# Performance work log

Hardware: AMD Instinct MI355X
Metric: run time of the kernel (lower is better)

## Reference

```python
import jax, jax.numpy as jnp
import numpy as np

N, B, C = 16384, 8, 256

def setup_inputs() -> dict:
    key = jax.random.key(0)
    k1, k2, k3, k4 = jax.random.split(key, 4)
    x = jax.random.normal(k1, (N, B, C), dtype=jnp.float32)
    mask = jax.random.randint(k2, (B, N), 0, 2, dtype=jnp.int32)      # 1 = padding
    fg_gt = jax.random.randint(k3, (N, B), 0, 2, dtype=jnp.int32)     # 1 = foreground gt
    W = jax.random.normal(k4, (C, C), dtype=jnp.float32) * (1.0 / np.sqrt(C))
    b = jnp.zeros((C,), dtype=jnp.float32)
    return {"x": x, "mask": mask, "fg_gt": fg_gt, "W": W, "b": b}

def reference(x, mask, fg_gt, W, b):
    # valid tokens: ~mask, permuted (B,N) -> (N,B)
    valid = (1 - mask.T).astype(x.dtype)                 # (N, B)
    m = (fg_gt != 0).astype(x.dtype) * valid             # gt_fg_token_mask, (N, B)
    # The per-batch gather -> Linear+ReLU -> scatter is equivalent to a
    # full batched GEMM followed by a masked select (linear is per-token).
    y = jax.nn.relu(jnp.einsum('nbc,dc->nbd', x, W) + b) # (N, B, C)
    x_new = x * (1.0 - m)[..., None] + y * m[..., None]
    return x_new, m
```

## Files before the change

kernel.cpp:

```cpp
#include <hip/hip_runtime.h>
#include <hip/hip_bf16.h>

#define N_TOK 16384
#define B_DIM 8
#define C_DIM 256
#define M_ROWS (N_TOK * B_DIM)
#define BM 32

typedef __attribute__((ext_vector_type(8))) short short8;
typedef __attribute__((ext_vector_type(4))) float f32x4;

__device__ __forceinline__ unsigned short f2bf(float f) {
    union { float f; unsigned u; } v; v.f = f;
    unsigned r = v.u + 0x7fffu + ((v.u >> 16) & 1u);
    return (unsigned short)(r >> 16);
}

__device__ __forceinline__ float bf2f(unsigned short h) {
    union { unsigned u; float f; } v; v.u = ((unsigned)h) << 16;
    return v.f;
}

__device__ __forceinline__ unsigned cvt_pk(float a, float b) {
    unsigned r;
    asm("v_cvt_pk_bf16_f32 %0, %1, %2" : "=v"(r) : "v"(a), "v"(b));
    return r;
}

__global__ __launch_bounds__(256)
void prep_kernel(const int* __restrict__ mask, const int* __restrict__ fg,
                 const float* __restrict__ W, unsigned short* __restrict__ Wf,
                 float* __restrict__ m_out) {
    int i = blockIdx.x * 256 + threadIdx.x;
    if (i < C_DIM * C_DIM) {
        int d = i >> 8;
        int c = i & 255;
        int ctile = d >> 4;
        int k8    = c >> 5;
        int lane  = ((c >> 3) & 3) * 16 + (d & 15);
        int r     = c & 7;
        Wf[((ctile * 8 + k8) * 64 + lane) * 8 + r] = f2bf(W[i]);
    }
    if (i < M_ROWS) {
        int b = i & (B_DIM - 1);
        int n = i >> 3;
        m_out[i] = (fg[i] != 0) ? (1.0f - (float)mask[b * N_TOK + n]) : 0.0f;
    }
}

__global__ __launch_bounds__(256, 6)
void mlp_kernel(const float* __restrict__ x, const unsigned short* __restrict__ Wf,
                const float* __restrict__ bias, const float* __restrict__ m,
                float* __restrict__ out) {
    __shared__ unsigned short lds_x[BM * C_DIM];

    const int t    = threadIdx.x;
    const int row0 = blockIdx.x * BM;

    #pragma unroll
    for (int j = 0; j < 4; ++j) {
        int ci  = j * 256 + t;
        int row = ci >> 5;
        int cc  = (ci & 31) * 8;
        const float4* p = (const float4*)(x + (size_t)(row0 + row) * C_DIM + cc);
        float4 a0 = p[0];
        float4 a1 = p[1];
        int4 pk;
        pk.x = (int)cvt_pk(a0.x, a0.y);
        pk.y = (int)cvt_pk(a0.z, a0.w);
        pk.z = (int)cvt_pk(a1.x, a1.y);
        pk.w = (int)cvt_pk(a1.z, a1.w);
        int byte = (row * 512 + cc * 2) ^ ((row & 7) << 4);
        *(int4*)((char*)lds_x + byte) = pk;
    }
    __syncthreads();

    const int lane = t & 63;
    const int wid  = t >> 6;
    const int col0 = wid * 64;
    const int lr   = lane & 15;
    const int kb   = (lane >> 4) * 8;
    const int rsub = (lane >> 4) * 4;

    f32x4 acc[2][4];
    #pragma unroll
    for (int i = 0; i < 2; ++i)
        #pragma unroll
        for (int j = 0; j < 4; ++j) acc[i][j] = (f32x4){0.f, 0.f, 0.f, 0.f};

    const short8* wfb = (const short8*)Wf + (size_t)wid * 4 * 8 * 64 + lane;

    #pragma unroll
    for (int k8 = 0; k8 < 8; ++k8) {
        short8 bf[4];
        #pragma unroll
        for (int ct = 0; ct < 4; ++ct)
            bf[ct] = wfb[(ct * 8 + k8) * 64];
        short8 af[2];
        #pragma unroll
        for (int rt = 0; rt < 2; ++rt) {
            int row  = rt * 16 + lr;
            int byte = (row * 512 + (k8 * 32 + kb) * 2) ^ ((row & 7) << 4);
            af[rt] = *(const short8*)((const char*)lds_x + byte);
        }
        #pragma unroll
        for (int rt = 0; rt < 2; ++rt)
            #pragma unroll
            for (int ct = 0; ct < 4; ++ct)
                acc[rt][ct] = __builtin_amdgcn_mfma_f32_16x16x32_bf16(
                    af[rt], bf[ct], acc[rt][ct], 0, 0, 0);
    }

    float bv[4];
    #pragma unroll
    for (int ct = 0; ct < 4; ++ct) bv[ct] = bias[col0 + ct * 16 + lr];

    #pragma unroll
    for (int rt = 0; rt < 2; ++rt) {
        float4 mreg = *(const float4*)(m + row0 + rt * 16 + rsub);
        #pragma unroll
        for (int r = 0; r < 4; ++r) {
            int lrow = rt * 16 + rsub + r;
            float mv = (r == 0) ? mreg.x : (r == 1) ? mreg.y
                     : (r == 2) ? mreg.z : mreg.w;
            size_t grow = (size_t)row0 + lrow;
            #pragma unroll
            for (int ct = 0; ct < 4; ++ct) {
                int col = col0 + ct * 16 + lr;
                float y = fmaxf(acc[rt][ct][r] + bv[ct], 0.0f);
                int bo = (lrow * 512 + col * 2) ^ ((lrow & 7) << 4);
                float xv = bf2f(*(const unsigned short*)((const char*)lds_x + bo));
                out[grow * C_DIM + col] = (mv != 0.0f) ? y : xv;
            }
        }
    }
}

extern "C" void kernel_launch(void* const* d_in, const int* in_sizes, int n_in,
                              void* d_out, int out_size, void* d_ws, size_t ws_size,
                              hipStream_t stream) {
    const float* x    = (const float*)d_in[0];
    const int*   mask = (const int*)d_in[1];
    const int*   fg   = (const int*)d_in[2];
    const float* W    = (const float*)d_in[3];
    const float* b    = (const float*)d_in[4];

    float* out   = (float*)d_out;
    float* m_out = out + (size_t)M_ROWS * C_DIM;
    unsigned short* Wf = (unsigned short*)d_ws;

    prep_kernel<<<M_ROWS / 256, 256, 0, stream>>>(mask, fg, W, Wf, m_out);
    mlp_kernel<<<M_ROWS / BM, 256, 0, stream>>>(x, Wf, b, m_out, out);
}
```

Measured before the change: 61.84 us.

## Make MLP kernel persistent with double-buffered direct-to-LDS loads and register-resident W

Each block now processes 8 row tiles with 512 threads. It keeps its slice of the bf16 weights in registers across tiles and prefetches the next tile of fp32 x into a second LDS buffer via global_load_lds while computing the current one. The fp32 tile is converted to bf16 at fragment-read time, and the passthrough value is read as exact fp32 from LDS. This aims to overlap HBM loads with MFMA and stores and to drop repeated weight reloads, at the cost of doubled LDS use and reliance on hand-tuned vmcnt waits.

```diff
diff --git a/kernel.cpp b/kernel.cpp
--- a/kernel.cpp
+++ b/kernel.cpp
@@ -6,6 +6,8 @@
 #define C_DIM 256
 #define M_ROWS (N_TOK * B_DIM)
 #define BM 32
+#define TPB 8
+#define GRID 512
 
 typedef __attribute__((ext_vector_type(8))) short short8;
 typedef __attribute__((ext_vector_type(4))) float f32x4;
@@ -16,15 +18,16 @@
     return (unsigned short)(r >> 16);
 }
 
-__device__ __forceinline__ float bf2f(unsigned short h) {
-    union { unsigned u; float f; } v; v.u = ((unsigned)h) << 16;
-    return v.f;
-}
-
 __device__ __forceinline__ unsigned cvt_pk(float a, float b) {
     unsigned r;
     asm("v_cvt_pk_bf16_f32 %0, %1, %2" : "=v"(r) : "v"(a), "v"(b));
     return r;
+}
+
+__device__ __forceinline__ void gload_lds16(const void* g, void* l) {
+    __builtin_amdgcn_global_load_lds(
+        (const __attribute__((address_space(1))) void*)g,
+        (__attribute__((address_space(3))) void*)l, 16, 0, 0);
 }
 
 __global__ __launch_bounds__(256)
@@ -48,91 +51,118 @@
     }
 }
 
-__global__ __launch_bounds__(256, 6)
+__global__ __launch_bounds__(512, 4)
 void mlp_kernel(const float* __restrict__ x, const unsigned short* __restrict__ Wf,
                 const float* __restrict__ bias, const float* __restrict__ m,
                 float* __restrict__ out) {
-    __shared__ unsigned short lds_x[BM * C_DIM];
+    __shared__ float lds[2][BM * C_DIM];
 
     const int t    = threadIdx.x;
-    const int row0 = blockIdx.x * BM;
-
-    #pragma unroll
-    for (int j = 0; j < 4; ++j) {
-        int ci  = j * 256 + t;
-        int row = ci >> 5;
-        int cc  = (ci & 31) * 8;
-        const float4* p = (const float4*)(x + (size_t)(row0 + row) * C_DIM + cc);
-        float4 a0 = p[0];
-        float4 a1 = p[1];
-        int4 pk;
-        pk.x = (int)cvt_pk(a0.x, a0.y);
-        pk.y = (int)cvt_pk(a0.z, a0.w);
-        pk.z = (int)cvt_pk(a1.x, a1.y);
-        pk.w = (int)cvt_pk(a1.z, a1.w);
-        int byte = (row * 512 + cc * 2) ^ ((row & 7) << 4);
-        *(int4*)((char*)lds_x + byte) = pk;
-    }
-    __syncthreads();
-
     const int lane = t & 63;
     const int wid  = t >> 6;
-    const int col0 = wid * 64;
     const int lr   = lane & 15;
     const int kb   = (lane >> 4) * 8;
     const int rsub = (lane >> 4) * 4;
 
-    f32x4 acc[2][4];
+    const int tile0 = blockIdx.x * TPB;
+
+    short8 wreg[2][8];
     #pragma unroll
-    for (int i = 0; i < 2; ++i)
+    for (int c2 = 0; c2 < 2; ++c2)
         #pragma unroll
-        for (int j = 0; j < 4; ++j) acc[i][j] = (f32x4){0.f, 0.f, 0.f, 0.f};
+        for (int k8 = 0; k8 < 8; ++k8)
+            wreg[c2][k8] = ((const short8*)Wf)[((wid * 2 + c2) * 8 + k8) * 64 + lane];
+    #pragma unroll
+    for (int c2 = 0; c2 < 2; ++c2)
+        #pragma unroll
+        for (int k8 = 0; k8 < 8; ++k8)
+            asm volatile("" : "+v"(wreg[c2][k8]));
 
-    const short8* wfb = (const short8*)Wf + (size_t)wid * 4 * 8 * 64 + lane;
+    float bv[2];
+    #pragma unroll
+    for (int c2 = 0; c2 < 2; ++c2) bv[c2] = bias[wid * 32 + c2 * 16 + lr];
 
-    #pragma unroll
-    for (int k8 = 0; k8 < 8; ++k8) {
-        short8 bf[4];
+    auto stage = [&](int buf, int tile) {
+        const char* xb = (const char*)x + (size_t)tile * BM * 1024;
         #pragma unroll
-        for (int ct = 0; ct < 4; ++ct)
-            bf[ct] = wfb[(ct * 8 + k8) * 64];
-        short8 af[2];
+        for (int r = 0; r < 4; ++r) {
+            int row = wid * 4 + r;
+            gload_lds16(xb + row * 1024 + ((lane * 16) ^ ((row & 7) << 4)),
+                        (char*)&lds[buf][0] + row * 1024);
+        }
+    };
+
+    float4 mA, mB, mA_n, mB_n;
+    stage(0, tile0);
+    mA = *(const float4*)(m + tile0 * BM + rsub);
+    mB = *(const float4*)(m + tile0 * BM + 16 + rsub);
+
+    for (int tt = 0; tt < TPB; ++tt) {
+        const int tile = tile0 + tt;
+        const int cur  = tt & 1;
+
+        if (tt == 0) asm volatile("s_waitcnt vmcnt(0)" ::: "memory");
+        else         asm volatile("s_waitcnt vmcnt(16)" ::: "memory");
+        __builtin_amdgcn_s_barrier();
+
+        if (tt + 1 < TPB) {
+            stage(cur ^ 1, tile + 1);
+            mA_n = *(const float4*)(m + (tile + 1) * BM + rsub);
+            mB_n = *(const float4*)(m + (tile + 1) * BM + 16 + rsub);
+        }
+
+        const char* Lc = (const char*)&lds[cur][0];
+        f32x4 acc[2][2];
+        #pragma unroll
+        for (int i = 0; i < 2; ++i)
+            #pragma unroll
+            for (int j = 0; j < 2; ++j) acc[i][j] = (f32x4){0.f, 0.f, 0.f, 0.f};
+
+        #pragma unroll
+        for (int k8 = 0; k8 < 8; ++k8) {
+            short8 af[2];
+            #pragma unroll
+            for (int rt = 0; rt < 2; ++rt) {
+                int row  = rt * 16 + lr;
+                int sz   = (row & 7) << 4;
+                int base = row * 1024 + (k8 * 32 + kb) * 4;
+                float4 f0 = *(const float4*)(Lc + (base ^ sz));
+                float4 f1 = *(const float4*)(Lc + ((base + 16) ^ sz));
+                int4 pk;
+                pk.x = (int)cvt_pk(f0.x, f0.y);
+                pk.y = (int)cvt_pk(f0.z, f0.w);
+                pk.z = (int)cvt_pk(f1.x, f1.y);
+                pk.w = (int)cvt_pk(f1.z, f1.w);
+                af[rt] = *(const short8*)&pk;
+            }
+            #pragma unroll
+            for (int rt = 0; rt < 2; ++rt)
+                #pragma unroll
+                for (int c2 = 0; c2 < 2; ++c2)
+                    acc[rt][c2] = __builtin_amdgcn_mfma_f32_16x16x32_bf16(
+                        af[rt], wreg[c2][k8], acc[rt][c2], 0, 0, 0);
+        }
+
         #pragma unroll
         for (int rt = 0; rt < 2; ++rt) {
-            int row  = rt * 16 + lr;
-            int byte = (row * 512 + (k8 * 32 + kb) * 2) ^ ((row & 7) << 4);
-            af[rt] = *(const short8*)((const char*)lds_x + byte);
-        }
-        #pragma unroll
-        for (int rt = 0; rt < 2; ++rt)
+            float4 mr = rt ? mB : mA;
             #pragma unroll
-            for (int ct = 0; ct < 4; ++ct)
-                acc[rt][ct] = __builtin_amdgcn_mfma_f32_16x16x32_bf16(
-                    af[rt], bf[ct], acc[rt][ct], 0, 0, 0);
-    }
-
-    float bv[4];
-    #pragma unroll
-    for (int ct = 0; ct < 4; ++ct) bv[ct] = bias[col0 + ct * 16 + lr];
-
-    #pragma unroll
-    for (int rt = 0; rt < 2; ++rt) {
-        float4 mreg = *(const float4*)(m + row0 + rt * 16 + rsub);
-        #pragma unroll
-        for (int r = 0; r < 4; ++r) {
-            int lrow = rt * 16 + rsub + r;
-            float mv = (r == 0) ? mreg.x : (r == 1) ? mreg.y
-                     : (r == 2) ? mreg.z : mreg.w;
-            size_t grow = (size_t)row0 + lrow;
-            #pragma unroll
-            for (int ct = 0; ct < 4; ++ct) {
-                int col = col0 + ct * 16 + lr;
-                float y = fmaxf(acc[rt][ct][r] + bv[ct], 0.0f);
-                int bo = (lrow * 512 + col * 2) ^ ((lrow & 7) << 4);
-                float xv = bf2f(*(const unsigned short*)((const char*)lds_x + bo));
-                out[grow * C_DIM + col] = (mv != 0.0f) ? y : xv;
+            for (int r = 0; r < 4; ++r) {
+                int lrow = rt * 16 + rsub + r;
+                float mv = (r == 0) ? mr.x : (r == 1) ? mr.y : (r == 2) ? mr.z : mr.w;
+                size_t grow = (size_t)tile * BM + lrow;
+                #pragma unroll
+                for (int c2 = 0; c2 < 2; ++c2) {
+                    int col = wid * 32 + c2 * 16 + lr;
+                    float y  = fmaxf(acc[rt][c2][r] + bv[c2], 0.0f);
+                    float xv = *(const float*)(Lc + ((lrow * 1024 + col * 4) ^ ((lrow & 7) << 4)));
+                    out[grow * C_DIM + col] = (mv != 0.0f) ? y : xv;
+                }
             }
         }
+
+        mA = mA_n; mB = mB_n;
+        __builtin_amdgcn_s_barrier();
     }
 }
 
@@ -150,5 +180,5 @@
     unsigned short* Wf = (unsigned short*)d_ws;
 
     prep_kernel<<<M_ROWS / 256, 256, 0, stream>>>(mask, fg, W, Wf, m_out);
-    mlp_kernel<<<M_ROWS / BM, 256, 0, stream>>>(x, Wf, b, m_out, out);
+    mlp_kernel<<<GRID, 512, 0, stream>>>(x, Wf, b, m_out, out);
 }
```

Result: slower. 143.9 us (+132.8%).

## Drop LDS staging of x; load A fragments directly from global with prefetch

Applied to the files above, without the earlier changes.

Removes the shared-memory tile of x and the block barrier. Each wave now loads its A fragments straight from global memory, converts them to bf16 in registers, and double-buffers both the x and W fragment loads across the k loop. The passthrough value in the epilogue is re-read from global x as fp32 instead of the bf16 LDS copy, which also restores exact passthrough values. The trade-off is that all four waves load the same x rows redundantly, adding global/L2 traffic and register pressure, so occupancy is lowered to 4 blocks.

```diff
diff --git a/kernel.cpp b/kernel.cpp
--- a/kernel.cpp
+++ b/kernel.cpp
@@ -14,11 +14,6 @@
     union { float f; unsigned u; } v; v.f = f;
     unsigned r = v.u + 0x7fffu + ((v.u >> 16) & 1u);
     return (unsigned short)(r >> 16);
-}
-
-__device__ __forceinline__ float bf2f(unsigned short h) {
-    union { unsigned u; float f; } v; v.u = ((unsigned)h) << 16;
-    return v.f;
 }
 
 __device__ __forceinline__ unsigned cvt_pk(float a, float b) {
@@ -48,39 +43,21 @@
     }
 }
 
-__global__ __launch_bounds__(256, 6)
+__global__ __launch_bounds__(256, 4)
 void mlp_kernel(const float* __restrict__ x, const unsigned short* __restrict__ Wf,
                 const float* __restrict__ bias, const float* __restrict__ m,
                 float* __restrict__ out) {
-    __shared__ unsigned short lds_x[BM * C_DIM];
-
     const int t    = threadIdx.x;
-    const int row0 = blockIdx.x * BM;
-
-    #pragma unroll
-    for (int j = 0; j < 4; ++j) {
-        int ci  = j * 256 + t;
-        int row = ci >> 5;
-        int cc  = (ci & 31) * 8;
-        const float4* p = (const float4*)(x + (size_t)(row0 + row) * C_DIM + cc);
-        float4 a0 = p[0];
-        float4 a1 = p[1];
-        int4 pk;
-        pk.x = (int)cvt_pk(a0.x, a0.y);
-        pk.y = (int)cvt_pk(a0.z, a0.w);
-        pk.z = (int)cvt_pk(a1.x, a1.y);
-        pk.w = (int)cvt_pk(a1.z, a1.w);
-        int byte = (row * 512 + cc * 2) ^ ((row & 7) << 4);
-        *(int4*)((char*)lds_x + byte) = pk;
-    }
-    __syncthreads();
-
     const int lane = t & 63;
     const int wid  = t >> 6;
+    const int lr   = lane & 15;
+    const int kq   = lane >> 4;
+    const int rsub = kq * 4;
+    const int row0 = blockIdx.x * BM;
     const int col0 = wid * 64;
-    const int lr   = lane & 15;
-    const int kb   = (lane >> 4) * 8;
-    const int rsub = (lane >> 4) * 4;
+
+    const char* xbA = (const char*)(x + (size_t)row0 * C_DIM) + lr * 1024 + kq * 32;
+    const short8* wf = (const short8*)Wf + lane;
 
     f32x4 acc[2][4];
     #pragma unroll
@@ -88,27 +65,53 @@
         #pragma unroll
         for (int j = 0; j < 4; ++j) acc[i][j] = (f32x4){0.f, 0.f, 0.f, 0.f};
 
-    const short8* wfb = (const short8*)Wf + (size_t)wid * 4 * 8 * 64 + lane;
+    float4 a_cur[2][2], a_nxt[2][2];
+    short8 w_cur[4], w_nxt[4];
+
+    #pragma unroll
+    for (int rt = 0; rt < 2; ++rt) {
+        a_cur[rt][0] = *(const float4*)(xbA + rt * 16384);
+        a_cur[rt][1] = *(const float4*)(xbA + rt * 16384 + 16);
+    }
+    #pragma unroll
+    for (int ct = 0; ct < 4; ++ct)
+        w_cur[ct] = wf[((wid * 4 + ct) * 8) * 64];
 
     #pragma unroll
     for (int k8 = 0; k8 < 8; ++k8) {
-        short8 bf[4];
-        #pragma unroll
-        for (int ct = 0; ct < 4; ++ct)
-            bf[ct] = wfb[(ct * 8 + k8) * 64];
+        if (k8 < 7) {
+            #pragma unroll
+            for (int rt = 0; rt < 2; ++rt) {
+                a_nxt[rt][0] = *(const float4*)(xbA + rt * 16384 + (k8 + 1) * 128);
+                a_nxt[rt][1] = *(const float4*)(xbA + rt * 16384 + (k8 + 1) * 128 + 16);
+            }
+            #pragma unroll
+            for (int ct = 0; ct < 4; ++ct)
+                w_nxt[ct] = wf[((wid * 4 + ct) * 8 + k8 + 1) * 64];
+        }
         short8 af[2];
         #pragma unroll
         for (int rt = 0; rt < 2; ++rt) {
-            int row  = rt * 16 + lr;
-            int byte = (row * 512 + (k8 * 32 + kb) * 2) ^ ((row & 7) << 4);
-            af[rt] = *(const short8*)((const char*)lds_x + byte);
+            int4 pk;
+            pk.x = (int)cvt_pk(a_cur[rt][0].x, a_cur[rt][0].y);
+            pk.y = (int)cvt_pk(a_cur[rt][0].z, a_cur[rt][0].w);
+            pk.z = (int)cvt_pk(a_cur[rt][1].x, a_cur[rt][1].y);
+            pk.w = (int)cvt_pk(a_cur[rt][1].z, a_cur[rt][1].w);
+            af[rt] = *(const short8*)&pk;
         }
         #pragma unroll
         for (int rt = 0; rt < 2; ++rt)
             #pragma unroll
             for (int ct = 0; ct < 4; ++ct)
                 acc[rt][ct] = __builtin_amdgcn_mfma_f32_16x16x32_bf16(
-                    af[rt], bf[ct], acc[rt][ct], 0, 0, 0);
+                    af[rt], w_cur[ct], acc[rt][ct], 0, 0, 0);
+        #pragma unroll
+        for (int rt = 0; rt < 2; ++rt) {
+            a_cur[rt][0] = a_nxt[rt][0];
+            a_cur[rt][1] = a_nxt[rt][1];
+        }
+        #pragma unroll
+        for (int ct = 0; ct < 4; ++ct) w_cur[ct] = w_nxt[ct];
     }
 
     float bv[4];
@@ -117,19 +120,17 @@
 
     #pragma unroll
     for (int rt = 0; rt < 2; ++rt) {
-        float4 mreg = *(const float4*)(m + row0 + rt * 16 + rsub);
+        float4 mr = *(const float4*)(m + row0 + rt * 16 + rsub);
         #pragma unroll
         for (int r = 0; r < 4; ++r) {
             int lrow = rt * 16 + rsub + r;
-            float mv = (r == 0) ? mreg.x : (r == 1) ? mreg.y
-                     : (r == 2) ? mreg.z : mreg.w;
+            float mv = (r == 0) ? mr.x : (r == 1) ? mr.y : (r == 2) ? mr.z : mr.w;
             size_t grow = (size_t)row0 + lrow;
             #pragma unroll
             for (int ct = 0; ct < 4; ++ct) {
                 int col = col0 + ct * 16 + lr;
-                float y = fmaxf(acc[rt][ct][r] + bv[ct], 0.0f);
-                int bo = (lrow * 512 + col * 2) ^ ((lrow & 7) << 4);
-                float xv = bf2f(*(const unsigned short*)((const char*)lds_x + bo));
+                float y  = fmaxf(acc[rt][ct][r] + bv[ct], 0.0f);
+                float xv = x[grow * C_DIM + col];
                 out[grow * C_DIM + col] = (mv != 0.0f) ? y : xv;
             }
         }
```

After: 103.4 us. +67.3%, slower.

## Split columns across block pairs, keep W in registers, prefetch second row tile

Applied to the files above, without the earlier changes.

Each block now processes 64 rows in two 32-row tiles but only half of the output columns, with a sibling block handling the other half. The block's weight slice is preloaded into registers, and the second tile's x data is fetched into registers while the first tile is computed, then staged into a second LDS buffer. This aims to hide global load latency and remove repeated weight loads from the inner loop. In exchange, each x row is read by two blocks, which raises global traffic unless the cache catches the duplicate reads, and register pressure grows.

```diff
diff --git a/kernel.cpp b/kernel.cpp
--- a/kernel.cpp
+++ b/kernel.cpp
@@ -5,7 +5,6 @@
 #define B_DIM 8
 #define C_DIM 256
 #define M_ROWS (N_TOK * B_DIM)
-#define BM 32
 
 typedef __attribute__((ext_vector_type(8))) short short8;
 typedef __attribute__((ext_vector_type(4))) float f32x4;
@@ -48,92 +47,145 @@
     }
 }
 
-__global__ __launch_bounds__(256, 6)
+__global__ __launch_bounds__(256)
 void mlp_kernel(const float* __restrict__ x, const unsigned short* __restrict__ Wf,
                 const float* __restrict__ bias, const float* __restrict__ m,
                 float* __restrict__ out) {
-    __shared__ unsigned short lds_x[BM * C_DIM];
+    __shared__ unsigned short lds_x[2][32 * C_DIM];
 
     const int t    = threadIdx.x;
-    const int row0 = blockIdx.x * BM;
+    const int lane = t & 63;
+    const int wid  = t >> 6;
+    const int half = blockIdx.x & 1;
+    const int row0 = (blockIdx.x >> 1) * 64;
+    const int col0 = half * 128 + wid * 32;
+    const int lr   = lane & 15;
+    const int kb   = (lane >> 4) * 8;
+    const int rsub = (lane >> 4) * 4;
+
+    short8 wreg[2][8];
+    const int ct0 = half * 8 + wid * 2;
+    #pragma unroll
+    for (int c2 = 0; c2 < 2; ++c2)
+        #pragma unroll
+        for (int k8 = 0; k8 < 8; ++k8)
+            wreg[c2][k8] = ((const short8*)Wf)[(size_t)((ct0 + c2) * 8 + k8) * 64 + lane];
+    #pragma unroll
+    for (int c2 = 0; c2 < 2; ++c2)
+        #pragma unroll
+        for (int k8 = 0; k8 < 8; ++k8)
+            asm volatile("" : "+v"(wreg[c2][k8]));
+
+    float bv[2];
+    bv[0] = bias[col0 + lr];
+    bv[1] = bias[col0 + 16 + lr];
+
+    f32x4 m00 = *(const f32x4*)(m + row0 + rsub);
+    f32x4 m01 = *(const f32x4*)(m + row0 + 16 + rsub);
+    f32x4 m10 = *(const f32x4*)(m + row0 + 32 + rsub);
+    f32x4 m11 = *(const f32x4*)(m + row0 + 48 + rsub);
 
     #pragma unroll
     for (int j = 0; j < 4; ++j) {
         int ci  = j * 256 + t;
         int row = ci >> 5;
         int cc  = (ci & 31) * 8;
-        const float4* p = (const float4*)(x + (size_t)(row0 + row) * C_DIM + cc);
-        float4 a0 = p[0];
-        float4 a1 = p[1];
+        const f32x4* p = (const f32x4*)(x + (size_t)(row0 + row) * C_DIM + cc);
+        f32x4 a0 = p[0];
+        f32x4 a1 = p[1];
         int4 pk;
         pk.x = (int)cvt_pk(a0.x, a0.y);
         pk.y = (int)cvt_pk(a0.z, a0.w);
         pk.z = (int)cvt_pk(a1.x, a1.y);
         pk.w = (int)cvt_pk(a1.z, a1.w);
         int byte = (row * 512 + cc * 2) ^ ((row & 7) << 4);
-        *(int4*)((char*)lds_x + byte) = pk;
-    }
-    __syncthreads();
-
-    const int lane = t & 63;
-    const int wid  = t >> 6;
-    const int col0 = wid * 64;
-    const int lr   = lane & 15;
-    const int kb   = (lane >> 4) * 8;
-    const int rsub = (lane >> 4) * 4;
-
-    f32x4 acc[2][4];
-    #pragma unroll
-    for (int i = 0; i < 2; ++i)
-        #pragma unroll
-        for (int j = 0; j < 4; ++j) acc[i][j] = (f32x4){0.f, 0.f, 0.f, 0.f};
-
-    const short8* wfb = (const short8*)Wf + (size_t)wid * 4 * 8 * 64 + lane;
-
-    #pragma unroll
-    for (int k8 = 0; k8 < 8; ++k8) {
-        short8 bf[4];
-        #pragma unroll
-        for (int ct = 0; ct < 4; ++ct)
-            bf[ct] = wfb[(ct * 8 + k8) * 64];
-        short8 af[2];
+        *(int4*)((char*)&lds_x[0][0] + byte) = pk;
+    }
+
+    const int r_  = t >> 5;
+    const int cc_ = (t & 31) * 8;
+    const float* xb1 = x + (size_t)(row0 + 32) * C_DIM;
+    f32x4 g0 = *(const f32x4*)(xb1 + (size_t)(r_     ) * C_DIM + cc_);
+    f32x4 g1 = *(const f32x4*)(xb1 + (size_t)(r_     ) * C_DIM + cc_ + 4);
+    f32x4 g2 = *(const f32x4*)(xb1 + (size_t)(r_ +  8) * C_DIM + cc_);
+    f32x4 g3 = *(const f32x4*)(xb1 + (size_t)(r_ +  8) * C_DIM + cc_ + 4);
+    f32x4 g4 = *(const f32x4*)(xb1 + (size_t)(r_ + 16) * C_DIM + cc_);
+    f32x4 g5 = *(const f32x4*)(xb1 + (size_t)(r_ + 16) * C_DIM + cc_ + 4);
+    f32x4 g6 = *(const f32x4*)(xb1 + (size_t)(r_ + 24) * C_DIM + cc_);
+    f32x4 g7 = *(const f32x4*)(xb1 + (size_t)(r_ + 24) * C_DIM + cc_ + 4);
+    __builtin_amdgcn_sched_barrier(0);
+
+    asm volatile("s_waitcnt lgkmcnt(0)" ::: "memory");
+    __builtin_amdgcn_s_barrier();
+    asm volatile("" ::: "memory");
+
+    auto do_tile = [&](const char* Lc, int trow0, f32x4 mA, f32x4 mB) {
+        f32x4 acc[2][2];
+        #pragma unroll
+        for (int i = 0; i < 2; ++i)
+            #pragma unroll
+            for (int j = 0; j < 2; ++j) acc[i][j] = (f32x4){0.f, 0.f, 0.f, 0.f};
+
+        #pragma unroll
+        for (int k8 = 0; k8 < 8; ++k8) {
+            short8 af[2];
+            #pragma unroll
+            for (int rt = 0; rt < 2; ++rt) {
+                int row  = rt * 16 + lr;
+                int byte = (row * 512 + (k8 * 32 + kb) * 2) ^ ((row & 7) << 4);
+                af[rt] = *(const short8*)(Lc + byte);
+            }
+            #pragma unroll
+            for (int rt = 0; rt < 2; ++rt)
+                #pragma unroll
+                for (int c2 = 0; c2 < 2; ++c2)
+                    acc[rt][c2] = __builtin_amdgcn_mfma_f32_16x16x32_bf16(
+                        af[rt], wreg[c2][k8], acc[rt][c2], 0, 0, 0);
+        }
+
         #pragma unroll
         for (int rt = 0; rt < 2; ++rt) {
-            int row  = rt * 16 + lr;
-            int byte = (row * 512 + (k8 * 32 + kb) * 2) ^ ((row & 7) << 4);
-            af[rt] = *(const short8*)((const char*)lds_x + byte);
-        }
-        #pragma unroll
-        for (int rt = 0; rt < 2; ++rt)
-            #pragma unroll
-            for (int ct = 0; ct < 4; ++ct)
-                acc[rt][ct] = __builtin_amdgcn_mfma_f32_16x16x32_bf16(
-                    af[rt], bf[ct], acc[rt][ct], 0, 0, 0);
-    }
-
-    float bv[4];
-    #pragma unroll
-    for (int ct = 0; ct < 4; ++ct) bv[ct] = bias[col0 + ct * 16 + lr];
-
-    #pragma unroll
-    for (int rt = 0; rt < 2; ++rt) {
-        float4 mreg = *(const float4*)(m + row0 + rt * 16 + rsub);
-        #pragma unroll
-        for (int r = 0; r < 4; ++r) {
-            int lrow = rt * 16 + rsub + r;
-            float mv = (r == 0) ? mreg.x : (r == 1) ? mreg.y
-                     : (r == 2) ? mreg.z : mreg.w;
-            size_t grow = (size_t)row0 + lrow;
-            #pragma unroll
-            for (int ct = 0; ct < 4; ++ct) {
-                int col = col0 + ct * 16 + lr;
-                float y = fmaxf(acc[rt][ct][r] + bv[ct], 0.0f);
-                int bo = (lrow * 512 + col * 2) ^ ((lrow & 7) << 4);
-                float xv = bf2f(*(const unsigned short*)((const char*)lds_x + bo));
-                out[grow * C_DIM + col] = (mv != 0.0f) ? y : xv;
+            f32x4 mr = rt ? mB : mA;
+            #pragma unroll
+            for (int r = 0; r < 4; ++r) {
+                int lrow = rt * 16 + rsub + r;
+                float mv = mr[r];
+                size_t grow = (size_t)trow0 + lrow;
+                #pragma unroll
+                for (int c2 = 0; c2 < 2; ++c2) {
+                    int col = col0 + c2 * 16 + lr;
+                    float y = fmaxf(acc[rt][c2][r] + bv[c2], 0.0f);
+                    int bo = (lrow * 512 + col * 2) ^ ((lrow & 7) << 4);
+                    float xv = bf2f(*(const unsigned short*)(Lc + bo));
+                    out[grow * C_DIM + col] = (mv != 0.0f) ? y : xv;
+                }
             }
         }
-    }
+    };
+
+    do_tile((const char*)&lds_x[0][0], row0, m00, m01);
+
+    {
+        int sz = (r_ & 7) << 4;
+        int4 pk;
+        pk.x = (int)cvt_pk(g0.x, g0.y); pk.y = (int)cvt_pk(g0.z, g0.w);
+        pk.z = (int)cvt_pk(g1.x, g1.y); pk.w = (int)cvt_pk(g1.z, g1.w);
+        *(int4*)((char*)&lds_x[1][0] + (((r_     ) * 512 + cc_ * 2) ^ sz)) = pk;
+        pk.x = (int)cvt_pk(g2.x, g2.y); pk.y = (int)cvt_pk(g2.z, g2.w);
+        pk.z = (int)cvt_pk(g3.x, g3.y); pk.w = (int)cvt_pk(g3.z, g3.w);
+        *(int4*)((char*)&lds_x[1][0] + (((r_ +  8) * 512 + cc_ * 2) ^ sz)) = pk;
+        pk.x = (int)cvt_pk(g4.x, g4.y); pk.y = (int)cvt_pk(g4.z, g4.w);
+        pk.z = (int)cvt_pk(g5.x, g5.y); pk.w = (int)cvt_pk(g5.z, g5.w);
+        *(int4*)((char*)&lds_x[1][0] + (((r_ + 16) * 512 + cc_ * 2) ^ sz)) = pk;
+        pk.x = (int)cvt_pk(g6.x, g6.y); pk.y = (int)cvt_pk(g6.z, g6.w);
+        pk.z = (int)cvt_pk(g7.x, g7.y); pk.w = (int)cvt_pk(g7.z, g7.w);
+        *(int4*)((char*)&lds_x[1][0] + (((r_ + 24) * 512 + cc_ * 2) ^ sz)) = pk;
+    }
+    asm volatile("s_waitcnt lgkmcnt(0)" ::: "memory");
+    __builtin_amdgcn_s_barrier();
+    asm volatile("" ::: "memory");
+
+    do_tile((const char*)&lds_x[1][0], row0 + 32, m10, m11);
 }
 
 extern "C" void kernel_launch(void* const* d_in, const int* in_sizes, int n_in,
@@ -150,5 +202,5 @@
     unsigned short* Wf = (unsigned short*)d_ws;
 
     prep_kernel<<<M_ROWS / 256, 256, 0, stream>>>(mask, fg, W, Wf, m_out);
-    mlp_kernel<<<M_ROWS / BM, 256, 0, stream>>>(x, Wf, b, m_out, out);
-}
+    mlp_kernel<<<(M_ROWS / 64) * 2, 256, 0, stream>>>(x, Wf, b, m_out, out);
+}
```

New measurement: 69.96 us. 13.1% more time.
